# Kernel optimization log

Hardware: AMD Instinct MI355X
Metric: run time of the kernel (lower is better)

## Reference

```python
import jax, jax.numpy as jnp
import numpy as np

N_NODES = 100000
N_EDGES = 3200000
IN_FEAT = 128
OUT_FEAT = 128
NUM_RELS = 16
NUM_BASES = 8


def setup_inputs() -> dict:
    key = jax.random.key(0)
    ks = jax.random.split(key, 7)
    x = jax.random.normal(ks[0], (N_NODES, IN_FEAT), dtype=jnp.float32)
    src = jax.random.randint(ks[1], (N_EDGES,), 0, N_NODES, dtype=jnp.int64)
    dst = jax.random.randint(ks[2], (N_EDGES,), 0, N_NODES, dtype=jnp.int64)
    etypes = jax.random.randint(ks[3], (N_EDGES,), 0, NUM_RELS, dtype=jnp.int64)
    # xavier_uniform with gain for relu = sqrt(2)
    gain = float(np.sqrt(2.0))
    limit_w = gain * float(np.sqrt(6.0 / (IN_FEAT + OUT_FEAT)))
    weight = jax.random.uniform(ks[4], (NUM_BASES, IN_FEAT, OUT_FEAT), dtype=jnp.float32,
                                minval=-limit_w, maxval=limit_w)
    limit_c = float(np.sqrt(6.0 / (NUM_RELS + NUM_BASES)))
    w_comp = jax.random.uniform(ks[5], (NUM_RELS, NUM_BASES), dtype=jnp.float32,
                                minval=-limit_c, maxval=limit_c)
    h_bias = jnp.zeros((OUT_FEAT,), dtype=jnp.float32)
    return {"x": x, "weight": weight, "w_comp": w_comp, "h_bias": h_bias,
            "src": src, "dst": dst, "etypes": etypes}


def reference(x, weight, w_comp, h_bias, src, dst, etypes):
    # basis decomposition: per-relation weight [R, in, out]
    W = jnp.einsum('rb,bio->rio', w_comp, weight)
    # transform all nodes under every relation: h[r, n, o]
    h = jnp.einsum('ni,rio->rno', x, W)
    # per-edge message = transformed source feature under the edge's relation type
    msg = h[etypes, src]  # [E, out]
    # scatter-sum messages into destination nodes
    node_repr = jax.ops.segment_sum(msg, dst, num_segments=N_NODES)
    node_repr = node_repr + h_bias
    return node_repr
```

## Files before the change

kernel.cpp:

```cpp
#include <hip/hip_runtime.h>
#include <hip/hip_bf16.h>
#include <stdint.h>

#define N_NODES   100000
#define N_EDGES   3200000
#define IN_FEAT   128
#define OUT_FEAT  128
#define NUM_RELS  16
#define NUM_BASES 8
#define M_PAD     100096
#define NBKT      391
#define NB        512

using short8 = __attribute__((ext_vector_type(8))) short;
using v4f    = __attribute__((ext_vector_type(4))) float;

__device__ inline unsigned short f2bf_rne(float f) {
    __hip_bfloat16 h = __float2bfloat16(f);
    return *reinterpret_cast<unsigned short*>(&h);
}
__device__ inline float bf2f(unsigned short u) {
    union { uint32_t i; float f; } x;
    x.i = ((uint32_t)u) << 16;
    return x.f;
}

__global__ void conv_x(const float* __restrict__ x, unsigned short* __restrict__ xb) {
    int id = blockIdx.x * 256 + threadIdx.x;
    int base = id * 4;
    ushort4 o;
    if (base < N_NODES * IN_FEAT) {
        const float4 v = reinterpret_cast<const float4*>(x)[id];
        o.x = f2bf_rne(v.x); o.y = f2bf_rne(v.y);
        o.z = f2bf_rne(v.z); o.w = f2bf_rne(v.w);
    } else {
        o.x = o.y = o.z = o.w = 0;
    }
    reinterpret_cast<ushort4*>(xb)[id] = o;
}

__global__ void build_ut(const float* __restrict__ weight,
                         unsigned short* __restrict__ Ut) {
    int id = blockIdx.x * 256 + threadIdx.x;
    int o  = id >> 10;
    int kk = id & 1023;
    int b  = kk >> 7;
    int i  = kk & 127;
    Ut[id] = f2bf_rne(weight[(b * IN_FEAT + i) * OUT_FEAT + o]);
}

__global__ __launch_bounds__(512) void coarse_hist(const int* __restrict__ dst,
                                                   int* __restrict__ histG,
                                                   int nbuck) {
    extern __shared__ int lh[];
    for (int i = threadIdx.x; i < nbuck; i += 512) lh[i] = 0;
    __syncthreads();
    const int NG = N_EDGES / 4;
    const int stride = NB * 512;
    for (int g = blockIdx.x * 512 + threadIdx.x; g < NG; g += stride) {
        const int4 d4 = reinterpret_cast<const int4*>(dst)[g];
        atomicAdd(&lh[d4.x >> 8], 1);
        atomicAdd(&lh[d4.y >> 8], 1);
        atomicAdd(&lh[d4.z >> 8], 1);
        atomicAdd(&lh[d4.w >> 8], 1);
    }
    __syncthreads();
    for (int i = threadIdx.x; i < nbuck; i += 512)
        histG[i * NB + blockIdx.x] = lh[i];
}

__global__ void scan_part(const int* __restrict__ data, int* __restrict__ partial, int K) {
    __shared__ int sh[256];
    const int tid = threadIdx.x, b = blockIdx.x;
    const int i0 = b * 4096 + tid * 16;
    int s = 0;
#pragma unroll
    for (int k = 0; k < 16; ++k) { int i = i0 + k; if (i < K) s += data[i]; }
    sh[tid] = s;
    __syncthreads();
    for (int st = 128; st > 0; st >>= 1) {
        if (tid < st) sh[tid] += sh[tid + st];
        __syncthreads();
    }
    if (tid == 0) partial[b] = sh[0];
}

__global__ __launch_bounds__(512) void scan_mid(int* __restrict__ partial, int G) {
    __shared__ int sh[512];
    const int tid = threadIdx.x;
    int v = (tid < G) ? partial[tid] : 0;
    sh[tid] = v;
    __syncthreads();
    for (int st = 1; st < 512; st <<= 1) {
        int t = (tid >= st) ? sh[tid - st] : 0;
        __syncthreads();
        sh[tid] += t;
        __syncthreads();
    }
    if (tid < G) partial[tid] = sh[tid] - v;
}

__global__ void scan_final(int* __restrict__ data, const int* __restrict__ partial, int K) {
    __shared__ int sh[256];
    const int tid = threadIdx.x, b = blockIdx.x;
    const int i0 = b * 4096 + tid * 16;
    int s = 0;
#pragma unroll
    for (int k = 0; k < 16; ++k) { int i = i0 + k; if (i < K) s += data[i]; }
    sh[tid] = s;
    __syncthreads();
    for (int st = 1; st < 256; st <<= 1) {
        int t = (tid >= st) ? sh[tid - st] : 0;
        __syncthreads();
        sh[tid] += t;
        __syncthreads();
    }
    int run = partial[b] + sh[tid] - s;
#pragma unroll
    for (int k = 0; k < 16; ++k) {
        int i = i0 + k;
        if (i < K) {
            int c = data[i];
            data[i] = run;
            run += c;
        }
    }
}

__global__ __launch_bounds__(512) void coarse_place(const int* __restrict__ src,
                                                    const int* __restrict__ dst,
                                                    const int* __restrict__ et,
                                                    const int* __restrict__ histS,
                                                    int* __restrict__ entries,
                                                    int nbuck) {
    extern __shared__ int cur[];
    for (int i = threadIdx.x; i < nbuck; i += 512)
        cur[i] = histS[i * NB + blockIdx.x];
    __syncthreads();
    const int NG = N_EDGES / 4;
    const int stride = NB * 512;
    for (int g = blockIdx.x * 512 + threadIdx.x; g < NG; g += stride) {
        const int4 s4 = reinterpret_cast<const int4*>(src)[g];
        const int4 d4 = reinterpret_cast<const int4*>(dst)[g];
        const int4 t4 = reinterpret_cast<const int4*>(et)[g];
        int p0 = atomicAdd(&cur[d4.x >> 8], 1);
        int p1 = atomicAdd(&cur[d4.y >> 8], 1);
        int p2 = atomicAdd(&cur[d4.z >> 8], 1);
        int p3 = atomicAdd(&cur[d4.w >> 8], 1);
        entries[p0] = ((d4.x & 255) << 21) | ((t4.x & 15) << 17) | s4.x;
        entries[p1] = ((d4.y & 255) << 21) | ((t4.y & 15) << 17) | s4.y;
        entries[p2] = ((d4.z & 255) << 21) | ((t4.z & 15) << 17) | s4.z;
        entries[p3] = ((d4.w & 255) << 21) | ((t4.w & 15) << 17) | s4.w;
    }
}

__global__ __launch_bounds__(256) void fine_sort(const int* __restrict__ entries,
                                                 const int* __restrict__ histS,
                                                 int* __restrict__ perm,
                                                 int* __restrict__ off,
                                                 int nbuck) {
    __shared__ int cnt[4096];
    __shared__ int bs[256];
    const int tid = threadIdx.x, b = blockIdx.x;
    const int start = histS[b * NB];
    const int end   = (b + 1 < nbuck) ? histS[(b + 1) * NB] : N_EDGES;

#pragma unroll
    for (int k = 0; k < 16; ++k) cnt[tid * 16 + k] = 0;
    __syncthreads();
    for (int i = start + tid; i < end; i += 256)
        atomicAdd(&cnt[entries[i] >> 17], 1);
    __syncthreads();

    int c[16];
    int tsum = 0;
#pragma unroll
    for (int k = 0; k < 16; ++k) { c[k] = cnt[tid * 16 + k]; tsum += c[k]; }
    bs[tid] = tsum;
    __syncthreads();
    for (int st = 1; st < 256; st <<= 1) {
        int t = (tid >= st) ? bs[tid - st] : 0;
        __syncthreads();
        bs[tid] += t;
        __syncthreads();
    }
    const int excl = bs[tid] - tsum;

    const int d = b * 256 + tid;
    if (d < N_NODES) off[d] = start + excl;
    if (b == nbuck - 1 && tid == 0) off[N_NODES] = N_EDGES;

    int run = excl;
#pragma unroll
    for (int k = 0; k < 16; ++k) { cnt[tid * 16 + k] = run; run += c[k]; }
    __syncthreads();
    for (int i = start + tid; i < end; i += 256) {
        int en = entries[i];
        int p = atomicAdd(&cnt[en >> 17], 1);
        perm[start + p] = en & 0x1FFFFF;
    }
}

__global__ void gather_z(const int* __restrict__ off, const int* __restrict__ perm,
                         const unsigned short* __restrict__ xb,
                         const float* __restrict__ w_comp,
                         unsigned short* __restrict__ zb) {
    __shared__ float csh[NUM_RELS * NUM_BASES];
    if (threadIdx.x < NUM_RELS * NUM_BASES) csh[threadIdx.x] = w_comp[threadIdx.x];
    __syncthreads();
    const int d = blockIdx.x * 4 + (threadIdx.x >> 6);
    const int lane = threadIdx.x & 63;
    float2 z[8];
#pragma unroll
    for (int b = 0; b < 8; ++b) z[b] = make_float2(0.f, 0.f);

    if (d < N_NODES) {
        const int e0 = off[d], e1 = off[d + 1];
        const unsigned short* xl = xb + lane * 2;
        int cur = -1;
        float2 srun = make_float2(0.f, 0.f);

        auto flush = [&]() {
            const float4 cA = *reinterpret_cast<const float4*>(&csh[cur * 8]);
            const float4 cB = *reinterpret_cast<const float4*>(&csh[cur * 8 + 4]);
            z[0].x += cA.x * srun.x; z[0].y += cA.x * srun.y;
            z[1].x += cA.y * srun.x; z[1].y += cA.y * srun.y;
            z[2].x += cA.z * srun.x; z[2].y += cA.z * srun.y;
            z[3].x += cA.w * srun.x; z[3].y += cA.w * srun.y;
            z[4].x += cB.x * srun.x; z[4].y += cB.x * srun.y;
            z[5].x += cB.y * srun.x; z[5].y += cB.y * srun.y;
            z[6].x += cB.z * srun.x; z[6].y += cB.z * srun.y;
            z[7].x += cB.w * srun.x; z[7].y += cB.w * srun.y;
        };
        auto step = [&](int p, ushort2 v) {
            int rl = p >> 17;
            if (rl != cur) {
                flush();
                cur = rl;
                srun = make_float2(0.f, 0.f);
            }
            srun.x += bf2f(v.x);
            srun.y += bf2f(v.y);
        };

        if (e0 < e1) {
            cur = perm[e0] >> 17;
            int e = e0;
            for (; e + 8 <= e1; e += 8) {
                int p[8];
#pragma unroll
                for (int j = 0; j < 8; ++j) p[j] = perm[e + j];
                ushort2 v[8];
#pragma unroll
                for (int j = 0; j < 8; ++j)
                    v[j] = *reinterpret_cast<const ushort2*>(
                        xl + (size_t)(p[j] & 0x1FFFF) * 128);
#pragma unroll
                for (int j = 0; j < 8; ++j) step(p[j], v[j]);
            }
            for (; e < e1; ++e) {
                int p = perm[e];
                ushort2 v = *reinterpret_cast<const ushort2*>(
                    xl + (size_t)(p & 0x1FFFF) * 128);
                step(p, v);
            }
            flush();
        }
    }

    unsigned short* zr = zb + (size_t)d * 1024 + lane * 2;
#pragma unroll
    for (int b = 0; b < 8; ++b) {
        unsigned int u = (unsigned int)f2bf_rne(z[b].x)
                       | ((unsigned int)f2bf_rne(z[b].y) << 16);
        __builtin_nontemporal_store(u, reinterpret_cast<unsigned int*>(zr + b * 128));
    }
}

__global__ __launch_bounds__(256, 2) void zgemm(const unsigned short* __restrict__ zb,
                                                const unsigned short* __restrict__ Ut,
                                                const float* __restrict__ bias,
                                                float* __restrict__ out) {
    __shared__ unsigned short lA[128 * 128];
    __shared__ unsigned short lB[128 * 128];

    const int mb = blockIdx.x;
    const int tid  = threadIdx.x;
    const int wid  = tid >> 6;
    const int lane = tid & 63;
    const int wm = wid >> 1, wn = wid & 1;
    const int ml = lane & 15, kgrp = lane >> 4;

    const unsigned short* gA = zb + (size_t)mb * 128 * 1024;

    v4f acc[4][4];
#pragma unroll
    for (int i = 0; i < 4; ++i)
#pragma unroll
        for (int j = 0; j < 4; ++j)
            acc[i][j] = (v4f){0.f, 0.f, 0.f, 0.f};

    for (int kt = 0; kt < 8; ++kt) {
#pragma unroll
        for (int it = 0; it < 8; ++it) {
            int sbase = it * 256 + wid * 64;
            int s = sbase + lane;
            int row = s >> 4;
            int cc = (s & 15) ^ (row & 15);
            __builtin_amdgcn_global_load_lds(
                (const __attribute__((address_space(1))) void*)(gA + (size_t)row * 1024 + kt * 128 + cc * 8),
                (__attribute__((address_space(3))) void*)(&lA[sbase * 8]), 16, 0, 0);
            __builtin_amdgcn_global_load_lds(
                (const __attribute__((address_space(1))) void*)(Ut + (size_t)row * 1024 + kt * 128 + cc * 8),
                (__attribute__((address_space(3))) void*)(&lB[sbase * 8]), 16, 0, 0);
        }
        __syncthreads();

#pragma unroll
        for (int kb = 0; kb < 4; ++kb) {
            const int cc = kb * 4 + kgrp;
            short8 af[4], bfr[4];
#pragma unroll
            for (int tm = 0; tm < 4; ++tm) {
                int rA = wm * 64 + tm * 16 + ml;
                af[tm] = *reinterpret_cast<const short8*>(&lA[(rA * 16 + (cc ^ (rA & 15))) * 8]);
            }
#pragma unroll
            for (int tn = 0; tn < 4; ++tn) {
                int rB = wn * 64 + tn * 16 + ml;
                bfr[tn] = *reinterpret_cast<const short8*>(&lB[(rB * 16 + (cc ^ (rB & 15))) * 8]);
            }
#pragma unroll
            for (int tm = 0; tm < 4; ++tm)
#pragma unroll
                for (int tn = 0; tn < 4; ++tn)
                    acc[tm][tn] = __builtin_amdgcn_mfma_f32_16x16x32_bf16(af[tm], bfr[tn], acc[tm][tn], 0, 0, 0);
        }
        __syncthreads();
    }

    const int row0 = mb * 128 + wm * 64;
    const int col0 = wn * 64;
#pragma unroll
    for (int tm = 0; tm < 4; ++tm)
#pragma unroll
        for (int rr = 0; rr < 4; ++rr) {
            int row = row0 + tm * 16 + kgrp * 4 + rr;
            if (row < N_NODES) {
                size_t rb = (size_t)row * OUT_FEAT;
#pragma unroll
                for (int tn = 0; tn < 4; ++tn) {
                    int col = col0 + tn * 16 + ml;
                    out[rb + col] = acc[tm][tn][rr] + bias[col];
                }
            }
        }
}

static inline size_t align256(size_t a) { return (a + 255) & ~(size_t)255; }

extern "C" void kernel_launch(void* const* d_in, const int* in_sizes, int n_in,
                              void* d_out, int out_size, void* d_ws, size_t ws_size,
                              hipStream_t stream) {
    const float* x      = (const float*)d_in[0];
    const float* weight = (const float*)d_in[1];
    const float* w_comp = (const float*)d_in[2];
    const float* h_bias = (const float*)d_in[3];
    const int*   src    = (const int*)d_in[4];
    const int*   dst    = (const int*)d_in[5];
    const int*   etypes = (const int*)d_in[6];
    float* out = (float*)d_out;

    const int nbuck = NBKT;
    const int K2 = nbuck * NB;
    const int G2 = (K2 + 4095) / 4096;

    size_t a = 512 * 1024;
    size_t xb_o = a;   a = align256(a + (size_t)M_PAD * 128 * 2);
    size_t perm_o = a; a = align256(a + (size_t)N_EDGES * 4);
    size_t off_o = a;  a = align256(a + ((size_t)N_NODES + 1) * 4);
    size_t part_o = a; a = align256(a + 512 * 4);
    size_t zb_o = a;

    char* w = (char*)d_ws;
    unsigned short* Ut      = (unsigned short*)(w);
    unsigned short* xb      = (unsigned short*)(w + xb_o);
    int*            perm    = (int*)(w + perm_o);
    int*            off     = (int*)(w + off_o);
    int*            partial = (int*)(w + part_o);
    unsigned short* zb      = (unsigned short*)(w + zb_o);
    int*            entries = (int*)(w + zb_o);
    int*            histG   = (int*)(w + zb_o + 13 * 1024 * 1024);

    conv_x<<<12512, 256, 0, stream>>>(x, xb);
    build_ut<<<512, 256, 0, stream>>>(weight, Ut);

    coarse_hist<<<NB, 512, nbuck * 4, stream>>>(dst, histG, nbuck);
    scan_part<<<G2, 256, 0, stream>>>(histG, partial, K2);
    scan_mid<<<1, 512, 0, stream>>>(partial, G2);
    scan_final<<<G2, 256, 0, stream>>>(histG, partial, K2);
    coarse_place<<<NB, 512, nbuck * 4, stream>>>(src, dst, etypes, histG, entries, nbuck);
    fine_sort<<<nbuck, 256, 0, stream>>>(entries, histG, perm, off, nbuck);

    gather_z<<<25024, 256, 0, stream>>>(off, perm, xb, w_comp, zb);
    zgemm<<<782, 256, 0, stream>>>(zb, Ut, h_bias, out);
}
```

Before: 415.3 us.

## Fuse preprocessing kernels, widen fine sort, pre-shift gather indices, drop nontemporal stores

Result: faster. 406.5 us (-2.1%).

```diff
diff --git a/kernel.cpp b/kernel.cpp
--- a/kernel.cpp
+++ b/kernel.cpp
@@ -25,48 +25,51 @@
     return x.f;
 }
 
-__global__ void conv_x(const float* __restrict__ x, unsigned short* __restrict__ xb) {
-    int id = blockIdx.x * 256 + threadIdx.x;
-    int base = id * 4;
-    ushort4 o;
-    if (base < N_NODES * IN_FEAT) {
-        const float4 v = reinterpret_cast<const float4*>(x)[id];
-        o.x = f2bf_rne(v.x); o.y = f2bf_rne(v.y);
-        o.z = f2bf_rne(v.z); o.w = f2bf_rne(v.w);
+__global__ __launch_bounds__(512) void fused_pre(const float* __restrict__ x,
+                                                 unsigned short* __restrict__ xb,
+                                                 const int* __restrict__ dst,
+                                                 int* __restrict__ histG,
+                                                 const float* __restrict__ weight,
+                                                 unsigned short* __restrict__ Ut,
+                                                 int nbuck) {
+    const int b = blockIdx.x;
+    if (b < 6256) {
+        int id = b * 512 + threadIdx.x;
+        int base = id * 4;
+        ushort4 o;
+        if (base < N_NODES * IN_FEAT) {
+            const float4 v = reinterpret_cast<const float4*>(x)[id];
+            o.x = f2bf_rne(v.x); o.y = f2bf_rne(v.y);
+            o.z = f2bf_rne(v.z); o.w = f2bf_rne(v.w);
+        } else {
+            o.x = o.y = o.z = o.w = 0;
+        }
+        reinterpret_cast<ushort4*>(xb)[id] = o;
+    } else if (b < 6256 + NB) {
+        extern __shared__ int lh[];
+        const int hb = b - 6256;
+        for (int i = threadIdx.x; i < nbuck; i += 512) lh[i] = 0;
+        __syncthreads();
+        const int NG = N_EDGES / 4;
+        const int stride = NB * 512;
+        for (int g = hb * 512 + threadIdx.x; g < NG; g += stride) {
+            const int4 d4 = reinterpret_cast<const int4*>(dst)[g];
+            atomicAdd(&lh[d4.x >> 8], 1);
+            atomicAdd(&lh[d4.y >> 8], 1);
+            atomicAdd(&lh[d4.z >> 8], 1);
+            atomicAdd(&lh[d4.w >> 8], 1);
+        }
+        __syncthreads();
+        for (int i = threadIdx.x; i < nbuck; i += 512)
+            histG[i * NB + hb] = lh[i];
     } else {
-        o.x = o.y = o.z = o.w = 0;
-    }
-    reinterpret_cast<ushort4*>(xb)[id] = o;
-}
-
-__global__ void build_ut(const float* __restrict__ weight,
-                         unsigned short* __restrict__ Ut) {
-    int id = blockIdx.x * 256 + threadIdx.x;
-    int o  = id >> 10;
-    int kk = id & 1023;
-    int b  = kk >> 7;
-    int i  = kk & 127;
-    Ut[id] = f2bf_rne(weight[(b * IN_FEAT + i) * OUT_FEAT + o]);
-}
-
-__global__ __launch_bounds__(512) void coarse_hist(const int* __restrict__ dst,
-                                                   int* __restrict__ histG,
-                                                   int nbuck) {
-    extern __shared__ int lh[];
-    for (int i = threadIdx.x; i < nbuck; i += 512) lh[i] = 0;
-    __syncthreads();
-    const int NG = N_EDGES / 4;
-    const int stride = NB * 512;
-    for (int g = blockIdx.x * 512 + threadIdx.x; g < NG; g += stride) {
-        const int4 d4 = reinterpret_cast<const int4*>(dst)[g];
-        atomicAdd(&lh[d4.x >> 8], 1);
-        atomicAdd(&lh[d4.y >> 8], 1);
-        atomicAdd(&lh[d4.z >> 8], 1);
-        atomicAdd(&lh[d4.w >> 8], 1);
-    }
-    __syncthreads();
-    for (int i = threadIdx.x; i < nbuck; i += 512)
-        histG[i * NB + blockIdx.x] = lh[i];
+        int id = (b - 6256 - NB) * 512 + threadIdx.x;
+        int o  = id >> 10;
+        int kk = id & 1023;
+        int bb = kk >> 7;
+        int i  = kk & 127;
+        Ut[id] = f2bf_rne(weight[(bb * IN_FEAT + i) * OUT_FEAT + o]);
+    }
 }
 
 __global__ void scan_part(const int* __restrict__ data, int* __restrict__ partial, int K) {
@@ -154,7 +157,7 @@
     }
 }
 
-__global__ __launch_bounds__(256) void fine_sort(const int* __restrict__ entries,
+__global__ __launch_bounds__(512) void fine_sort(const int* __restrict__ entries,
                                                  const int* __restrict__ histS,
                                                  int* __restrict__ perm,
                                                  int* __restrict__ off,
@@ -165,39 +168,41 @@
     const int start = histS[b * NB];
     const int end   = (b + 1 < nbuck) ? histS[(b + 1) * NB] : N_EDGES;
 
-#pragma unroll
-    for (int k = 0; k < 16; ++k) cnt[tid * 16 + k] = 0;
-    __syncthreads();
-    for (int i = start + tid; i < end; i += 256)
+    for (int i = tid; i < 4096; i += 512) cnt[i] = 0;
+    __syncthreads();
+    for (int i = start + tid; i < end; i += 512)
         atomicAdd(&cnt[entries[i] >> 17], 1);
     __syncthreads();
 
     int c[16];
     int tsum = 0;
-#pragma unroll
-    for (int k = 0; k < 16; ++k) { c[k] = cnt[tid * 16 + k]; tsum += c[k]; }
-    bs[tid] = tsum;
+    if (tid < 256) {
+#pragma unroll
+        for (int k = 0; k < 16; ++k) { c[k] = cnt[tid * 16 + k]; tsum += c[k]; }
+        bs[tid] = tsum;
+    }
     __syncthreads();
     for (int st = 1; st < 256; st <<= 1) {
-        int t = (tid >= st) ? bs[tid - st] : 0;
-        __syncthreads();
-        bs[tid] += t;
-        __syncthreads();
-    }
-    const int excl = bs[tid] - tsum;
-
-    const int d = b * 256 + tid;
-    if (d < N_NODES) off[d] = start + excl;
+        int t = 0;
+        if (tid < 256 && tid >= st) t = bs[tid - st];
+        __syncthreads();
+        if (tid < 256) bs[tid] += t;
+        __syncthreads();
+    }
+    if (tid < 256) {
+        const int excl = bs[tid] - tsum;
+        const int d = b * 256 + tid;
+        if (d < N_NODES) off[d] = start + excl;
+        int run = excl;
+#pragma unroll
+        for (int k = 0; k < 16; ++k) { cnt[tid * 16 + k] = run; run += c[k]; }
+    }
     if (b == nbuck - 1 && tid == 0) off[N_NODES] = N_EDGES;
-
-    int run = excl;
-#pragma unroll
-    for (int k = 0; k < 16; ++k) { cnt[tid * 16 + k] = run; run += c[k]; }
-    __syncthreads();
-    for (int i = start + tid; i < end; i += 256) {
+    __syncthreads();
+    for (int i = start + tid; i < end; i += 512) {
         int en = entries[i];
         int p = atomicAdd(&cnt[en >> 17], 1);
-        perm[start + p] = en & 0x1FFFFF;
+        perm[start + p] = ((en & 0x1FFFF) << 8) | ((en >> 17) & 15);
     }
 }
 
@@ -216,7 +221,7 @@
 
     if (d < N_NODES) {
         const int e0 = off[d], e1 = off[d + 1];
-        const unsigned short* xl = xb + lane * 2;
+        const char* xB = (const char*)xb + lane * 4;
         int cur = -1;
         float2 srun = make_float2(0.f, 0.f);
 
@@ -233,7 +238,7 @@
             z[7].x += cB.w * srun.x; z[7].y += cB.w * srun.y;
         };
         auto step = [&](int p, ushort2 v) {
-            int rl = p >> 17;
+            int rl = p & 15;
             if (rl != cur) {
                 flush();
                 cur = rl;
@@ -244,7 +249,7 @@
         };
 
         if (e0 < e1) {
-            cur = perm[e0] >> 17;
+            cur = perm[e0] & 15;
             int e = e0;
             for (; e + 8 <= e1; e += 8) {
                 int p[8];
@@ -254,14 +259,14 @@
 #pragma unroll
                 for (int j = 0; j < 8; ++j)
                     v[j] = *reinterpret_cast<const ushort2*>(
-                        xl + (size_t)(p[j] & 0x1FFFF) * 128);
+                        xB + (uint32_t)(p[j] & 0x01FFFF00));
 #pragma unroll
                 for (int j = 0; j < 8; ++j) step(p[j], v[j]);
             }
             for (; e < e1; ++e) {
                 int p = perm[e];
                 ushort2 v = *reinterpret_cast<const ushort2*>(
-                    xl + (size_t)(p & 0x1FFFF) * 128);
+                    xB + (uint32_t)(p & 0x01FFFF00));
                 step(p, v);
             }
             flush();
@@ -273,7 +278,7 @@
     for (int b = 0; b < 8; ++b) {
         unsigned int u = (unsigned int)f2bf_rne(z[b].x)
                        | ((unsigned int)f2bf_rne(z[b].y) << 16);
-        __builtin_nontemporal_store(u, reinterpret_cast<unsigned int*>(zr + b * 128));
+        *reinterpret_cast<unsigned int*>(zr + b * 128) = u;
     }
 }
 
@@ -392,15 +397,13 @@
     int*            entries = (int*)(w + zb_o);
     int*            histG   = (int*)(w + zb_o + 13 * 1024 * 1024);
 
-    conv_x<<<12512, 256, 0, stream>>>(x, xb);
-    build_ut<<<512, 256, 0, stream>>>(weight, Ut);
-
-    coarse_hist<<<NB, 512, nbuck * 4, stream>>>(dst, histG, nbuck);
+    fused_pre<<<6256 + NB + 256, 512, nbuck * 4, stream>>>(x, xb, dst, histG,
+                                                           weight, Ut, nbuck);
     scan_part<<<G2, 256, 0, stream>>>(histG, partial, K2);
     scan_mid<<<1, 512, 0, stream>>>(partial, G2);
     scan_final<<<G2, 256, 0, stream>>>(histG, partial, K2);
     coarse_place<<<NB, 512, nbuck * 4, stream>>>(src, dst, etypes, histG, entries, nbuck);
-    fine_sort<<<nbuck, 256, 0, stream>>>(entries, histG, perm, off, nbuck);
+    fine_sort<<<nbuck, 512, 0, stream>>>(entries, histG, perm, off, nbuck);
 
     gather_z<<<25024, 256, 0, stream>>>(off, perm, xb, w_comp, zb);
     zgemm<<<782, 256, 0, stream>>>(zb, Ut, h_bias, out);
```
